# Optimization experiments

Hardware: AMD Instinct MI355X
Metric: run time of the kernel (lower is better)

Reference implementation:

```python
import jax, jax.numpy as jnp
import numpy as np

TOP_K = 2
EPS = 1e-10


def setup_inputs() -> dict:
    key = jax.random.key(0)
    k1, k2, k3, k4 = jax.random.split(key, 4)
    B, S, H, E = 4, 2048, 1024, 8
    tokens = jax.random.normal(k1, (B, S, H), dtype=jnp.float32)
    router_w = jax.random.normal(k2, (E, H), dtype=jnp.float32) * (1.0 / np.sqrt(H))
    router_b = jax.random.normal(k3, (E,), dtype=jnp.float32) * 0.01
    expert_weights = jax.random.normal(k4, (E, H, H), dtype=jnp.float32) * (1.0 / np.sqrt(H))
    return {"tokens": tokens, "router_w": router_w, "router_b": router_b,
            "expert_weights": expert_weights}


def reference(tokens, router_w, router_b, expert_weights):
    B, S, H = tokens.shape
    E = expert_weights.shape[0]
    # Router (torch Linear: x @ W^T + b)
    logits = jnp.einsum('bsh,eh->bse', tokens, router_w) + router_b  # [B,S,E]
    probs = jax.nn.softmax(logits, axis=-1)
    top_p, top_i = jax.lax.top_k(probs, TOP_K)            # [B,S,K]
    w = top_p / (jnp.sum(top_p, axis=-1, keepdims=True) + EPS)  # normalized weights

    x = tokens.reshape(-1, H)                              # [N,H]
    idx = top_i.reshape(-1, TOP_K)                         # [N,K]
    wf = w.reshape(-1, TOP_K)                              # [N,K]

    # Expert GEMM: compute all experts then gather selected (dense, vectorized
    # equivalent of the sort/pad/grouped-GEMM dispatch; padded rows with
    # original_indices==-1 never contribute to the output).
    y_all = jnp.einsum('nh,ehd->ned', x, expert_weights)   # [N,E,H]
    y_k = jnp.take_along_axis(y_all, idx[:, :, None], axis=1)  # [N,K,H]

    out = jnp.einsum('nk,nkh->nh', wf, y_k)                # weighted combine
    acc = jnp.clip(jnp.sum(wf, axis=-1), EPS, None)        # weight accumulator
    out = (out / acc[:, None]).reshape(B, S, H)

    # epsilon scale tying output to normalized router probs (gradient path)
    scale = 1.0 + jnp.sum(w, axis=-1, keepdims=True) * EPS  # [B,S,1]
    return out * scale
```

## Files before the change

### kernel.cpp

```cpp
#include <hip/hip_runtime.h>
#include <stdint.h>

#define N_TOK 8192
#define H_DIM 1024
#define N_EXP 8
#define GEMM_GRID 1024

typedef __bf16 bf16x8 __attribute__((ext_vector_type(8)));
typedef float floatx4 __attribute__((ext_vector_type(4)));

typedef __attribute__((address_space(1))) void GV;
typedef __attribute__((address_space(3))) void LV;

static __device__ __forceinline__ unsigned short f2b(float f) {
    union { float f; unsigned int i; } v; v.f = f;
    unsigned int u = v.i;
    return (unsigned short)((u + 0x7FFFu + ((u >> 16) & 1u)) >> 16);
}
static __device__ __forceinline__ float b2f(unsigned short u) {
    union { unsigned int i; float f; } v; v.i = ((unsigned int)u) << 16; return v.f;
}

__global__ __launch_bounds__(256) void k_front(
    const float* __restrict__ tokens,
    const float* __restrict__ router_w,
    const float* __restrict__ router_b,
    const float* __restrict__ W,
    int* __restrict__ sel, float* __restrict__ w_arr,
    unsigned short* __restrict__ tokb,
    unsigned short* __restrict__ Bp)
{
    const int t = threadIdx.x;

    if (blockIdx.x >= 2048) {
        const int idx = blockIdx.x - 2048;
        const int kg = idx & 127;
        const int e  = idx >> 7;
        const int d  = t * 4;
        const float* src = W + ((size_t)e * H_DIM + kg * 8) * H_DIM + d;
        float col[8][4];
#pragma unroll
        for (int j = 0; j < 8; ++j) {
            float4 v = *(const float4*)(src + (size_t)j * H_DIM);
            col[j][0] = v.x; col[j][1] = v.y; col[j][2] = v.z; col[j][3] = v.w;
        }
        unsigned short* dst = Bp + ((size_t)(e * 128 + kg) * H_DIM + d) * 8;
#pragma unroll
        for (int k = 0; k < 4; ++k) {
            unsigned short v[8];
#pragma unroll
            for (int j = 0; j < 8; ++j) v[j] = f2b(col[j][k]);
            *(uint4*)(dst + (size_t)k * 8) = *(uint4*)v;
        }
        return;
    }

    const int wave = t >> 6;
    const int lane = t & 63;
    const int n = blockIdx.x * 4 + wave;

    const float* xp = tokens + (size_t)n * H_DIM + lane * 16;
    float x[16];
#pragma unroll
    for (int i = 0; i < 4; ++i) {
        float4 v = *(const float4*)(xp + i * 4);
        x[i * 4 + 0] = v.x; x[i * 4 + 1] = v.y; x[i * 4 + 2] = v.z; x[i * 4 + 3] = v.w;
    }

    {
        unsigned short xb[16];
#pragma unroll
        for (int j = 0; j < 16; ++j) xb[j] = f2b(x[j]);
        unsigned short* dp = tokb + (size_t)n * H_DIM + lane * 16;
        *(uint4*)(dp)     = *(uint4*)(xb);
        *(uint4*)(dp + 8) = *(uint4*)(xb + 8);
    }

    float acc[N_EXP];
#pragma unroll
    for (int e = 0; e < N_EXP; ++e) {
        const float* wp = router_w + e * H_DIM + lane * 16;
        float s = 0.f;
#pragma unroll
        for (int i = 0; i < 4; ++i) {
            float4 v = *(const float4*)(wp + i * 4);
            s += x[i * 4 + 0] * v.x + x[i * 4 + 1] * v.y
               + x[i * 4 + 2] * v.z + x[i * 4 + 3] * v.w;
        }
        acc[e] = s;
    }

#pragma unroll
    for (int e = 0; e < N_EXP; ++e) {
        float a = acc[e];
#pragma unroll
        for (int off = 32; off > 0; off >>= 1) a += __shfl_xor(a, off);
        acc[e] = a;
    }

    if (lane == 0) {
        float lg[N_EXP];
#pragma unroll
        for (int e = 0; e < N_EXP; ++e) lg[e] = acc[e] + router_b[e];
        int e0 = 0;
#pragma unroll
        for (int e = 1; e < N_EXP; ++e) if (lg[e] > lg[e0]) e0 = e;
        int e1 = -1;
#pragma unroll
        for (int e = 0; e < N_EXP; ++e) {
            if (e == e0) continue;
            if (e1 < 0 || lg[e] > lg[e1]) e1 = e;
        }
        float w0 = 1.f / (1.f + __expf(lg[e1] - lg[e0]));
        float w1 = 1.f - w0;
        sel[n] = e0 | (e1 << 4);
        w_arr[n * 2] = w0;
        w_arr[n * 2 + 1] = w1;
    }
}

__global__ __launch_bounds__(256) void k_scan(
    const int* __restrict__ sel, int* __restrict__ cnt, int* __restrict__ bucket)
{
    __shared__ int ssel[N_TOK + N_TOK / 32];
    __shared__ int sc[256];
    const int e = blockIdx.x;
    const int t = threadIdx.x;
#pragma unroll
    for (int i = 0; i < 32; ++i) {
        int n = i * 256 + t;
        ssel[n + (n >> 5)] = sel[n];
    }
    __syncthreads();
    const int base = t * 32;
    int c = 0;
#pragma unroll
    for (int i = 0; i < 32; ++i) {
        int n = base + i;
        int s = ssel[n + (n >> 5)];
        c += ((s & 15) == e) + (((s >> 4) & 15) == e);
    }
    sc[t] = c;
    __syncthreads();
    for (int off = 1; off < 256; off <<= 1) {
        int v = (t >= off) ? sc[t - off] : 0;
        __syncthreads();
        sc[t] += v;
        __syncthreads();
    }
    int pos = sc[t] - c;
    if (t == 255) cnt[e] = sc[255];
#pragma unroll
    for (int i = 0; i < 32; ++i) {
        int n = base + i;
        int s = ssel[n + (n >> 5)];
        if ((s & 15) == e)        bucket[e * N_TOK + pos++] = 2 * n;
        if (((s >> 4) & 15) == e) bucket[e * N_TOK + pos++] = 2 * n + 1;
    }
}

__global__ __launch_bounds__(256, 4) void k_gemm(
    const unsigned short* __restrict__ tokb,
    const unsigned short* __restrict__ Bp,
    const int* __restrict__ cnt, const int* __restrict__ bucket,
    unsigned short* __restrict__ Y)
{
    __shared__ __align__(16) unsigned short Asm[128 * 64];
    __shared__ __align__(16) unsigned short Bsm[8 * 128 * 8];
    __shared__ int rows[128];

    const int t = threadIdx.x;
    const int wv = t >> 6, lane = t & 63;
    const int w_row = wv >> 1, w_col = wv & 1;
    const int m_lane = lane & 15, quad = lane >> 4;
    const int r7 = m_lane & 7;
    const int p_sw = (lane & 7) ^ ((lane >> 3) & 7);

    int cs[N_EXP];
#pragma unroll
    for (int ee = 0; ee < N_EXP; ++ee) cs[ee] = cnt[ee];
    int T = 0;
#pragma unroll
    for (int ee = 0; ee < N_EXP; ++ee) T += (cs[ee] + 127) >> 7;

    const int x = blockIdx.x & 7;
    const int sblk = blockIdx.x >> 3;
    const int q = T >> 3, r = T & 7;
    const int tstart = (x < r) ? x * (q + 1) : r * (q + 1) + (x - r) * q;
    const int tcnt   = (x < r) ? (q + 1) : q;
    const int nloc   = tcnt * 8;

    for (int l = sblk; l < nloc; l += 128) {
        const int tile = tstart + (l >> 3);
        const int nt   = l & 7;
        int base = 0, e = 0, mt = 0;
#pragma unroll
        for (int ee = 0; ee < N_EXP; ++ee) {
            int te = (cs[ee] + 127) >> 7;
            if (tile >= base && tile < base + te) { e = ee; mt = tile - base; }
            base += te;
        }
        const int cnt_local = cs[e] - mt * 128;
        const int d0 = nt * 128;

        __syncthreads();
        if (t < 128)
            rows[t] = (t < cnt_local) ? bucket[e * N_TOK + mt * 128 + t] : -1;
        __syncthreads();

        const unsigned short* aptr[4];
#pragma unroll
        for (int i = 0; i < 4; ++i) {
            int rr = i * 32 + wv * 8 + (lane >> 3);
            int rid = rows[rr];
            int tok = (rid >= 0) ? (rid >> 1) : 0;
            aptr[i] = tokb + (size_t)tok * H_DIM + p_sw * 8;
        }
        const unsigned short* bbase = Bp
            + ((size_t)(e * 128 + (t >> 7)) * H_DIM + d0 + (t & 127)) * 8;

        floatx4 acc[4][4];
#pragma unroll
        for (int i = 0; i < 4; ++i)
#pragma unroll
            for (int j = 0; j < 4; ++j) acc[i][j] = (floatx4){0.f, 0.f, 0.f, 0.f};

        for (int kt = 0; kt < H_DIM / 64; ++kt) {
#pragma unroll
            for (int i = 0; i < 4; ++i) {
                __builtin_amdgcn_global_load_lds(
                    (GV*)(aptr[i] + kt * 64),
                    (LV*)(&Asm[i * 2048 + wv * 512]), 16, 0, 0);
                __builtin_amdgcn_global_load_lds(
                    (GV*)(bbase + (size_t)i * 16384 + (size_t)kt * 65536),
                    (LV*)(&Bsm[i * 2048 + wv * 512]), 16, 0, 0);
            }
            __syncthreads();

#pragma unroll
            for (int s = 0; s < 2; ++s) {
                bf16x8 a[4], b[4];
#pragma unroll
                for (int i = 0; i < 4; ++i) {
                    int row = w_row * 64 + i * 16 + m_lane;
                    a[i] = *(const bf16x8*)&Asm[row * 64 + ((s * 4 + quad) ^ r7) * 8];
                }
#pragma unroll
                for (int j = 0; j < 4; ++j)
                    b[j] = *(const bf16x8*)&Bsm[((s * 4 + quad) * 128 + w_col * 64 + j * 16 + m_lane) * 8];
#pragma unroll
                for (int i = 0; i < 4; ++i)
#pragma unroll
                    for (int j = 0; j < 4; ++j)
                        acc[i][j] = __builtin_amdgcn_mfma_f32_16x16x32_bf16(a[i], b[j], acc[i][j], 0, 0, 0);
            }
            __syncthreads();
        }

#pragma unroll
        for (int i = 0; i < 4; ++i) {
            const int lr_base = w_row * 64 + i * 16 + quad * 4;
#pragma unroll
            for (int reg = 0; reg < 4; ++reg) {
                const int lr = lr_base + reg;
                const int rid = rows[lr];
                if (rid >= 0) {
                    unsigned short v[4];
#pragma unroll
                    for (int j = 0; j < 4; ++j) v[j] = f2b(acc[i][j][reg]);
                    *(uint2*)(Y + (size_t)rid * H_DIM + d0 + w_col * 64 + m_lane * 4) = *(uint2*)v;
                }
            }
        }
    }
}

__global__ __launch_bounds__(256) void k_combine(
    const unsigned short* __restrict__ Y, const float* __restrict__ w_arr,
    float* __restrict__ out)
{
    __shared__ __align__(16) unsigned short Ys[4 * H_DIM];
    const int t = threadIdx.x;
    const int b = blockIdx.x;
    const int wv = t >> 6, lane = t & 63;
    const unsigned short* src = Y + (size_t)b * 4 * H_DIM;
#pragma unroll
    for (int r = 0; r < 2; ++r) {
        __builtin_amdgcn_global_load_lds(
            (GV*)(src + (size_t)r * 2048 + wv * 512 + lane * 8),
            (LV*)(&Ys[r * 2048 + wv * 512]), 16, 0, 0);
    }
    __syncthreads();

    const int tok = t >> 7;
    const int n = 2 * b + tok;
    const int d0 = (t & 127) * 8;
    const int seg = d0 >> 7;
    const int dseg = d0 & 127;
    const int wc = dseg >> 6;
    const int j  = (dseg >> 4) & 3;
    const int m0 = dseg & 15;
    const int sbase = tok * 2 * H_DIM + seg * 128 + wc * 64 + j;
    const float w0 = w_arr[2 * n], w1 = w_arr[2 * n + 1];

    float o[8];
#pragma unroll
    for (int k = 0; k < 8; ++k) {
        int s = sbase + (m0 + k) * 4;
        o[k] = w0 * b2f(Ys[s]) + w1 * b2f(Ys[s + H_DIM]);
    }
    float4* op = (float4*)(out + (size_t)n * H_DIM + d0);
    op[0] = make_float4(o[0], o[1], o[2], o[3]);
    op[1] = make_float4(o[4], o[5], o[6], o[7]);
}

extern "C" void kernel_launch(void* const* d_in, const int* in_sizes, int n_in,
                              void* d_out, int out_size, void* d_ws, size_t ws_size,
                              hipStream_t stream)
{
    const float* tokens   = (const float*)d_in[0];
    const float* router_w = (const float*)d_in[1];
    const float* router_b = (const float*)d_in[2];
    const float* W        = (const float*)d_in[3];
    float* out = (float*)d_out;

    char* ws = (char*)d_ws;
    int*   cnt    = (int*)(ws);
    int*   sel    = (int*)(ws + 1024);
    float* w_arr  = (float*)(ws + 34816);
    int*   bucket = (int*)(ws + 100352);
    unsigned short* tokb = (unsigned short*)(ws + 362496);
    unsigned short* Bp   = (unsigned short*)(ws + 17139712);
    unsigned short* Y    = (unsigned short*)(ws + 33916928);

    k_front  <<<2048 + 1024, 256, 0, stream>>>(tokens, router_w, router_b, W,
                                               sel, w_arr, tokb, Bp);
    k_scan   <<<N_EXP, 256, 0, stream>>>(sel, cnt, bucket);
    k_gemm   <<<GEMM_GRID, 256, 0, stream>>>(tokb, Bp, cnt, bucket, Y);
    k_combine<<<N_TOK * (H_DIM / 8) / 256, 256, 0, stream>>>(Y, w_arr, out);
}
```

Measured before the change: 186.3 us.

## Double-buffer GEMM LDS tiles with K=32 steps to overlap loads with MFMA

Changes the grouped expert GEMM main loop from single-buffered K=64 tiles to double-buffered K=32 tiles. The next tile's global-to-LDS loads are issued before the current tile's MFMAs, so each iteration needs one barrier instead of two. The A-tile swizzle is reworked for the narrower 32-wide rows. This is meant to hide global load latency behind compute, at the cost of twice as many iterations with fewer MFMAs between barriers.

```diff
diff --git a/kernel.cpp b/kernel.cpp
--- a/kernel.cpp
+++ b/kernel.cpp
@@ -165,16 +165,16 @@
     const int* __restrict__ cnt, const int* __restrict__ bucket,
     unsigned short* __restrict__ Y)
 {
-    __shared__ __align__(16) unsigned short Asm[128 * 64];
-    __shared__ __align__(16) unsigned short Bsm[8 * 128 * 8];
+    __shared__ __align__(16) unsigned short Asm[2][128 * 32];
+    __shared__ __align__(16) unsigned short Bsm[2][4 * 128 * 8];
     __shared__ int rows[128];
 
     const int t = threadIdx.x;
     const int wv = t >> 6, lane = t & 63;
     const int w_row = wv >> 1, w_col = wv & 1;
     const int m_lane = lane & 15, quad = lane >> 4;
-    const int r7 = m_lane & 7;
-    const int p_sw = (lane & 7) ^ ((lane >> 3) & 7);
+    const int aslot = quad ^ (m_lane & 3) ^ ((m_lane >> 2) & 3);
+    const int p_sw = (t & 3) ^ ((t >> 2) & 3) ^ ((t >> 4) & 3);
 
     int cs[N_EXP];
 #pragma unroll
@@ -208,16 +208,13 @@
             rows[t] = (t < cnt_local) ? bucket[e * N_TOK + mt * 128 + t] : -1;
         __syncthreads();
 
-        const unsigned short* aptr[4];
-#pragma unroll
-        for (int i = 0; i < 4; ++i) {
-            int rr = i * 32 + wv * 8 + (lane >> 3);
-            int rid = rows[rr];
-            int tok = (rid >= 0) ? (rid >> 1) : 0;
-            aptr[i] = tokb + (size_t)tok * H_DIM + p_sw * 8;
-        }
-        const unsigned short* bbase = Bp
-            + ((size_t)(e * 128 + (t >> 7)) * H_DIM + d0 + (t & 127)) * 8;
+        const int r0 = t >> 2;
+        const int rid0 = rows[r0], rid1 = rows[64 + r0];
+        const unsigned short* aptr0 = tokb + (size_t)((rid0 >= 0) ? (rid0 >> 1) : 0) * H_DIM + p_sw * 8;
+        const unsigned short* aptr1 = tokb + (size_t)((rid1 >= 0) ? (rid1 >> 1) : 0) * H_DIM + p_sw * 8;
+        const int kgt = t >> 7;
+        const unsigned short* bb0 = Bp + ((size_t)(e * 128 + kgt)     * H_DIM + d0 + (t & 127)) * 8;
+        const unsigned short* bb1 = Bp + ((size_t)(e * 128 + 2 + kgt) * H_DIM + d0 + (t & 127)) * 8;
 
         floatx4 acc[4][4];
 #pragma unroll
@@ -225,35 +222,41 @@
 #pragma unroll
             for (int j = 0; j < 4; ++j) acc[i][j] = (floatx4){0.f, 0.f, 0.f, 0.f};
 
-        for (int kt = 0; kt < H_DIM / 64; ++kt) {
+        __builtin_amdgcn_global_load_lds((GV*)aptr0, (LV*)(&Asm[0][wv * 512]), 16, 0, 0);
+        __builtin_amdgcn_global_load_lds((GV*)aptr1, (LV*)(&Asm[0][2048 + wv * 512]), 16, 0, 0);
+        __builtin_amdgcn_global_load_lds((GV*)bb0,   (LV*)(&Bsm[0][wv * 512]), 16, 0, 0);
+        __builtin_amdgcn_global_load_lds((GV*)bb1,   (LV*)(&Bsm[0][2048 + wv * 512]), 16, 0, 0);
+        __syncthreads();
+
+        for (int kt = 0; kt < H_DIM / 32; ++kt) {
+            const int cb = kt & 1;
+            if (kt < H_DIM / 32 - 1) {
+                const int kn = kt + 1;
+                __builtin_amdgcn_global_load_lds(
+                    (GV*)(aptr0 + kn * 32), (LV*)(&Asm[cb ^ 1][wv * 512]), 16, 0, 0);
+                __builtin_amdgcn_global_load_lds(
+                    (GV*)(aptr1 + kn * 32), (LV*)(&Asm[cb ^ 1][2048 + wv * 512]), 16, 0, 0);
+                __builtin_amdgcn_global_load_lds(
+                    (GV*)(bb0 + (size_t)kn * 32768), (LV*)(&Bsm[cb ^ 1][wv * 512]), 16, 0, 0);
+                __builtin_amdgcn_global_load_lds(
+                    (GV*)(bb1 + (size_t)kn * 32768), (LV*)(&Bsm[cb ^ 1][2048 + wv * 512]), 16, 0, 0);
+            }
+
+            bf16x8 a[4], b[4];
 #pragma unroll
             for (int i = 0; i < 4; ++i) {
-                __builtin_amdgcn_global_load_lds(
-                    (GV*)(aptr[i] + kt * 64),
-                    (LV*)(&Asm[i * 2048 + wv * 512]), 16, 0, 0);
-                __builtin_amdgcn_global_load_lds(
-                    (GV*)(bbase + (size_t)i * 16384 + (size_t)kt * 65536),
-                    (LV*)(&Bsm[i * 2048 + wv * 512]), 16, 0, 0);
+                int row = w_row * 64 + i * 16 + m_lane;
+                a[i] = *(const bf16x8*)&Asm[cb][row * 32 + aslot * 8];
             }
-            __syncthreads();
-
-#pragma unroll
-            for (int s = 0; s < 2; ++s) {
-                bf16x8 a[4], b[4];
-#pragma unroll
-                for (int i = 0; i < 4; ++i) {
-                    int row = w_row * 64 + i * 16 + m_lane;
-                    a[i] = *(const bf16x8*)&Asm[row * 64 + ((s * 4 + quad) ^ r7) * 8];
-                }
+#pragma unroll
+            for (int j = 0; j < 4; ++j)
+                b[j] = *(const bf16x8*)&Bsm[cb][(quad * 128 + w_col * 64 + j * 16 + m_lane) * 8];
+#pragma unroll
+            for (int i = 0; i < 4; ++i)
 #pragma unroll
                 for (int j = 0; j < 4; ++j)
-                    b[j] = *(const bf16x8*)&Bsm[((s * 4 + quad) * 128 + w_col * 64 + j * 16 + m_lane) * 8];
-#pragma unroll
-                for (int i = 0; i < 4; ++i)
-#pragma unroll
-                    for (int j = 0; j < 4; ++j)
-                        acc[i][j] = __builtin_amdgcn_mfma_f32_16x16x32_bf16(a[i], b[j], acc[i][j], 0, 0, 0);
-            }
+                    acc[i][j] = __builtin_amdgcn_mfma_f32_16x16x32_bf16(a[i], b[j], acc[i][j], 0, 0, 0);
+
             __syncthreads();
         }
 
```

After: 201.8 us. 8.3% more time.

## Fuse expert bucketing into router kernel with block-local lists and atomics

Applied to the files above, without the earlier changes.

Removes the separate scan kernel by building per-block expert lists in shared memory inside the router kernel and appending them to global buckets with atomicAdd on a zeroed counter array. Each wave now routes two tokens, halving router blocks and sharing router weight loads. The front kernel's grid shrinks from 3072 to 2048 blocks. This saves a launch and the serial 8-block scan, but adds a memset and makes bucket order nondeterministic, so GEMM row ordering varies between runs.

```diff
diff --git a/kernel.cpp b/kernel.cpp
--- a/kernel.cpp
+++ b/kernel.cpp
@@ -26,14 +26,15 @@
     const float* __restrict__ router_w,
     const float* __restrict__ router_b,
     const float* __restrict__ W,
-    int* __restrict__ sel, float* __restrict__ w_arr,
+    float* __restrict__ w_arr,
     unsigned short* __restrict__ tokb,
-    unsigned short* __restrict__ Bp)
+    unsigned short* __restrict__ Bp,
+    int* __restrict__ cnt, int* __restrict__ bucket)
 {
     const int t = threadIdx.x;
 
-    if (blockIdx.x >= 2048) {
-        const int idx = blockIdx.x - 2048;
+    if (blockIdx.x >= 1024) {
+        const int idx = blockIdx.x - 1024;
         const int kg = idx & 127;
         const int e  = idx >> 7;
         const int d  = t * 4;
@@ -55,107 +56,89 @@
         return;
     }
 
-    const int wave = t >> 6;
-    const int lane = t & 63;
-    const int n = blockIdx.x * 4 + wave;
-
-    const float* xp = tokens + (size_t)n * H_DIM + lane * 16;
-    float x[16];
+    __shared__ int bcnt[N_EXP];
+    __shared__ int blist[N_EXP][16];
+    if (t < N_EXP) bcnt[t] = 0;
+    __syncthreads();
+
+    const int wv = t >> 6, lane = t & 63;
+    const int n0 = blockIdx.x * 8 + wv * 2;
+
+    float x0[16], x1[16];
+    const float* xp0 = tokens + (size_t)n0 * H_DIM + lane * 16;
+    const float* xp1 = xp0 + H_DIM;
 #pragma unroll
     for (int i = 0; i < 4; ++i) {
-        float4 v = *(const float4*)(xp + i * 4);
-        x[i * 4 + 0] = v.x; x[i * 4 + 1] = v.y; x[i * 4 + 2] = v.z; x[i * 4 + 3] = v.w;
-    }
-
+        float4 v = *(const float4*)(xp0 + i * 4);
+        x0[i * 4 + 0] = v.x; x0[i * 4 + 1] = v.y; x0[i * 4 + 2] = v.z; x0[i * 4 + 3] = v.w;
+        float4 u = *(const float4*)(xp1 + i * 4);
+        x1[i * 4 + 0] = u.x; x1[i * 4 + 1] = u.y; x1[i * 4 + 2] = u.z; x1[i * 4 + 3] = u.w;
+    }
     {
         unsigned short xb[16];
 #pragma unroll
-        for (int j = 0; j < 16; ++j) xb[j] = f2b(x[j]);
-        unsigned short* dp = tokb + (size_t)n * H_DIM + lane * 16;
-        *(uint4*)(dp)     = *(uint4*)(xb);
-        *(uint4*)(dp + 8) = *(uint4*)(xb + 8);
-    }
-
-    float acc[N_EXP];
+        for (int j = 0; j < 16; ++j) xb[j] = f2b(x0[j]);
+        unsigned short* dp = tokb + (size_t)n0 * H_DIM + lane * 16;
+        *(uint4*)(dp) = *(uint4*)(xb); *(uint4*)(dp + 8) = *(uint4*)(xb + 8);
+#pragma unroll
+        for (int j = 0; j < 16; ++j) xb[j] = f2b(x1[j]);
+        dp += H_DIM;
+        *(uint4*)(dp) = *(uint4*)(xb); *(uint4*)(dp + 8) = *(uint4*)(xb + 8);
+    }
+
+    float a0[N_EXP], a1[N_EXP];
 #pragma unroll
     for (int e = 0; e < N_EXP; ++e) {
         const float* wp = router_w + e * H_DIM + lane * 16;
-        float s = 0.f;
+        float s0 = 0.f, s1 = 0.f;
 #pragma unroll
         for (int i = 0; i < 4; ++i) {
             float4 v = *(const float4*)(wp + i * 4);
-            s += x[i * 4 + 0] * v.x + x[i * 4 + 1] * v.y
-               + x[i * 4 + 2] * v.z + x[i * 4 + 3] * v.w;
-        }
-        acc[e] = s;
-    }
-
+            s0 += x0[i * 4 + 0] * v.x + x0[i * 4 + 1] * v.y + x0[i * 4 + 2] * v.z + x0[i * 4 + 3] * v.w;
+            s1 += x1[i * 4 + 0] * v.x + x1[i * 4 + 1] * v.y + x1[i * 4 + 2] * v.z + x1[i * 4 + 3] * v.w;
+        }
+        a0[e] = s0; a1[e] = s1;
+    }
 #pragma unroll
     for (int e = 0; e < N_EXP; ++e) {
-        float a = acc[e];
-#pragma unroll
-        for (int off = 32; off > 0; off >>= 1) a += __shfl_xor(a, off);
-        acc[e] = a;
+        float p = a0[e], q = a1[e];
+#pragma unroll
+        for (int off = 32; off > 0; off >>= 1) { p += __shfl_xor(p, off); q += __shfl_xor(q, off); }
+        a0[e] = p; a1[e] = q;
     }
 
     if (lane == 0) {
-        float lg[N_EXP];
-#pragma unroll
-        for (int e = 0; e < N_EXP; ++e) lg[e] = acc[e] + router_b[e];
-        int e0 = 0;
-#pragma unroll
-        for (int e = 1; e < N_EXP; ++e) if (lg[e] > lg[e0]) e0 = e;
-        int e1 = -1;
-#pragma unroll
-        for (int e = 0; e < N_EXP; ++e) {
-            if (e == e0) continue;
-            if (e1 < 0 || lg[e] > lg[e1]) e1 = e;
-        }
-        float w0 = 1.f / (1.f + __expf(lg[e1] - lg[e0]));
-        float w1 = 1.f - w0;
-        sel[n] = e0 | (e1 << 4);
-        w_arr[n * 2] = w0;
-        w_arr[n * 2 + 1] = w1;
-    }
-}
-
-__global__ __launch_bounds__(256) void k_scan(
-    const int* __restrict__ sel, int* __restrict__ cnt, int* __restrict__ bucket)
-{
-    __shared__ int ssel[N_TOK + N_TOK / 32];
-    __shared__ int sc[256];
-    const int e = blockIdx.x;
-    const int t = threadIdx.x;
-#pragma unroll
-    for (int i = 0; i < 32; ++i) {
-        int n = i * 256 + t;
-        ssel[n + (n >> 5)] = sel[n];
+#pragma unroll
+        for (int k = 0; k < 2; ++k) {
+            const int n = n0 + k;
+            float lg[N_EXP];
+#pragma unroll
+            for (int e = 0; e < N_EXP; ++e) lg[e] = (k ? a1[e] : a0[e]) + router_b[e];
+            int e0 = 0;
+#pragma unroll
+            for (int e = 1; e < N_EXP; ++e) if (lg[e] > lg[e0]) e0 = e;
+            int e1 = -1;
+#pragma unroll
+            for (int e = 0; e < N_EXP; ++e) {
+                if (e == e0) continue;
+                if (e1 < 0 || lg[e] > lg[e1]) e1 = e;
+            }
+            float w0 = 1.f / (1.f + __expf(lg[e1] - lg[e0]));
+            w_arr[n * 2] = w0;
+            w_arr[n * 2 + 1] = 1.f - w0;
+            int s0 = atomicAdd(&bcnt[e0], 1); blist[e0][s0] = 2 * n;
+            int s1 = atomicAdd(&bcnt[e1], 1); blist[e1][s1] = 2 * n + 1;
+        }
     }
     __syncthreads();
-    const int base = t * 32;
-    int c = 0;
-#pragma unroll
-    for (int i = 0; i < 32; ++i) {
-        int n = base + i;
-        int s = ssel[n + (n >> 5)];
-        c += ((s & 15) == e) + (((s >> 4) & 15) == e);
-    }
-    sc[t] = c;
-    __syncthreads();
-    for (int off = 1; off < 256; off <<= 1) {
-        int v = (t >= off) ? sc[t - off] : 0;
-        __syncthreads();
-        sc[t] += v;
-        __syncthreads();
-    }
-    int pos = sc[t] - c;
-    if (t == 255) cnt[e] = sc[255];
-#pragma unroll
-    for (int i = 0; i < 32; ++i) {
-        int n = base + i;
-        int s = ssel[n + (n >> 5)];
-        if ((s & 15) == e)        bucket[e * N_TOK + pos++] = 2 * n;
-        if (((s >> 4) & 15) == e) bucket[e * N_TOK + pos++] = 2 * n + 1;
+
+    if (t < N_EXP) {
+        int c = bcnt[t];
+        if (c > 0) {
+            int base = atomicAdd(&cnt[t], c);
+            int* dst = bucket + t * N_TOK + base;
+            for (int i = 0; i < c; ++i) dst[i] = blist[t][i];
+        }
     }
 }
 
@@ -326,16 +309,15 @@
 
     char* ws = (char*)d_ws;
     int*   cnt    = (int*)(ws);
-    int*   sel    = (int*)(ws + 1024);
     float* w_arr  = (float*)(ws + 34816);
     int*   bucket = (int*)(ws + 100352);
     unsigned short* tokb = (unsigned short*)(ws + 362496);
     unsigned short* Bp   = (unsigned short*)(ws + 17139712);
     unsigned short* Y    = (unsigned short*)(ws + 33916928);
 
-    k_front  <<<2048 + 1024, 256, 0, stream>>>(tokens, router_w, router_b, W,
-                                               sel, w_arr, tokb, Bp);
-    k_scan   <<<N_EXP, 256, 0, stream>>>(sel, cnt, bucket);
+    hipMemsetAsync(cnt, 0, N_EXP * sizeof(int), stream);
+    k_front  <<<2048, 256, 0, stream>>>(tokens, router_w, router_b, W,
+                                        w_arr, tokb, Bp, cnt, bucket);
     k_gemm   <<<GEMM_GRID, 256, 0, stream>>>(tokb, Bp, cnt, bucket, Y);
     k_combine<<<N_TOK * (H_DIM / 8) / 256, 256, 0, stream>>>(Y, w_arr, out);
 }
```

Result: faster. 178.6 us (-4.1%).
